# Optimization experiments

Hardware: AMD Instinct MI355X
Metric: run time of the kernel (lower is better)

The kernel has to match this reference:

```python
import jax, jax.numpy as jnp
import numpy as np

NUM_CLASSES = 10

def setup_inputs() -> dict:
    key = jax.random.key(0)
    k1, k2, k3 = jax.random.split(key, 3)
    X = jax.random.normal(k1, (1024, 128), dtype=jnp.float32)
    X_train = jax.random.normal(k2, (100000, 128), dtype=jnp.float32)
    y_train = jax.random.randint(k3, (100000,), 0, NUM_CLASSES, dtype=jnp.int64)
    return {"X": X, "X_train": X_train, "y_train": y_train, "k": 5}


def reference(X, X_train, y_train, k):
    test_sq = jnp.sum(X * X, axis=1, keepdims=True)            # [T, 1]
    train_sq = jnp.sum(X_train * X_train, axis=1)[None, :]     # [1, N]
    cross = X @ X_train.T                                      # [T, N]
    dists = jnp.sqrt(jnp.maximum(test_sq + train_sq - 2.0 * cross, 0.0))
    # top-k nearest: smallest distances == largest negated distances
    _, idx = jax.lax.top_k(-dists, k)                          # [T, k]
    labels = y_train[idx]                                      # [T, k]
    # majority vote; argmax returns the smallest label on ties,
    # matching most_frq_smaller semantics
    counts = jnp.sum(jax.nn.one_hot(labels, NUM_CLASSES, dtype=jnp.int32), axis=1)  # [T, C]
    y_pred = jnp.argmax(counts, axis=1).astype(jnp.float32)    # torch.zeros default float
    return y_pred
```

## Files before the change

kernel.cpp:

```cpp
#include <hip/hip_runtime.h>
#include <cfloat>
#include <cstdint>


#define NTRAIN 100000
#define D 128
#define T 1024
#define TB 128
#define NT 32
#define KNN 5
#define NUM_CLASSES 10
#define NCH 125
#define CHUNK 800
#define NSUB 32
#define SCHUNK 224
#define NTILE_TOT 3125
#define TILE_HALVES 8192

typedef _Float16 half8 __attribute__((ext_vector_type(8)));
typedef float f32x16 __attribute__((ext_vector_type(16)));

#define MFMA(a, b, c) __builtin_amdgcn_mfma_f32_32x32x16_f16((a), (b), (c), 0, 0, 0)

struct Cand { float s; int j; };

__device__ __forceinline__ bool better(float s, int j, const Cand& c) {
    return (s > c.s) || (s == c.s && j < c.j);
}

__device__ __forceinline__ void ins5(Cand t5[KNN], float s, int j) {
    if (!better(s, j, t5[4])) return;
    if (better(s, j, t5[0]))      { t5[4]=t5[3]; t5[3]=t5[2]; t5[2]=t5[1]; t5[1]=t5[0]; t5[0]={s,j}; }
    else if (better(s, j, t5[1])) { t5[4]=t5[3]; t5[3]=t5[2]; t5[2]=t5[1]; t5[1]={s,j}; }
    else if (better(s, j, t5[2])) { t5[4]=t5[3]; t5[3]=t5[2]; t5[2]={s,j}; }
    else if (better(s, j, t5[3])) { t5[4]=t5[3]; t5[3]={s,j}; }
    else                          { t5[4]={s,j}; }
}

__device__ __forceinline__ void gload_lds16(const void* g, void* l) {
    __builtin_amdgcn_global_load_lds(
        (const __attribute__((address_space(1))) uint32_t*)g,
        (__attribute__((address_space(3))) uint32_t*)l, 16, 0, 0);
}

__global__ __launch_bounds__(256)
void knn_norms(const float* __restrict__ XT, uint32_t* __restrict__ nrmp) {
    const int j = blockIdx.x * 256 + threadIdx.x;
    if (j >= NTRAIN) return;
    const float4* row = (const float4*)&XT[(size_t)j * D];
    float p[32];
#pragma unroll
    for (int c = 0; c < 32; ++c) {
        float4 v = row[c];
        p[c] = v.x * v.x + v.y * v.y + v.z * v.z + v.w * v.w;
    }
#pragma unroll
    for (int s = 1; s < 32; s <<= 1)
#pragma unroll
        for (int i = 0; i < 32; i += 2 * s) p[i] += p[i + s];
    const float m = -0.5f * p[0];
    const _Float16 mh = (_Float16)m;
    const _Float16 ml = (_Float16)(m - (float)mh);
    union { _Float16 h[2]; uint32_t u; } cv;
    cv.h[0] = mh; cv.h[1] = ml;
    nrmp[j] = cv.u;
}

__global__ __launch_bounds__(256)
void knn_pack(const float* __restrict__ XT, _Float16* __restrict__ XTs,
              uint32_t* __restrict__ nrmp) {
    __shared__ __align__(16) float sb[32 * D];
    const int tid  = threadIdx.x;
    const int tile = blockIdx.x;
    const float4* src = (const float4*)&XT[(size_t)tile * 32 * D];
#pragma unroll
    for (int p = 0; p < 4; ++p)
        *(float4*)&sb[(p * 256 + tid) * 4] = src[p * 256 + tid];
    __syncthreads();

    {
        const int ks = tid >> 5, kh = (tid >> 4) & 1, rp = (tid & 15) * 2;
        const int c0 = ks * 16 + kh * 8;
        _Float16* outp = &XTs[(size_t)tile * TILE_HALVES + tid * 16];
#pragma unroll
        for (int rr = 0; rr < 2; ++rr) {
            const float* s = &sb[(rp + rr) * D + c0];
            half8 hv, lv;
#pragma unroll
            for (int e = 0; e < 8; ++e) {
                float v = s[e];
                _Float16 hh = (_Float16)v;
                hv[e] = hh; lv[e] = (_Float16)(v - (float)hh);
            }
            *(half8*)&outp[rr * 8]        = hv;
            *(half8*)&outp[4096 + rr * 8] = lv;
        }
    }
    {
        const int row = tid >> 3, seg = tid & 7;
        const float4* rp4 = (const float4*)&sb[row * D];
        float q[4];
#pragma unroll
        for (int c = 0; c < 4; ++c) {
            float4 v = rp4[seg * 4 + c];
            q[c] = v.x * v.x + v.y * v.y + v.z * v.z + v.w * v.w;
        }
        float part = (q[0] + q[1]) + (q[2] + q[3]);
        part += __shfl_xor(part, 1);
        part += __shfl_xor(part, 2);
        part += __shfl_xor(part, 4);
        if (seg == 0) {
            const float m = -0.5f * part;
            const _Float16 mh = (_Float16)m;
            const _Float16 ml = (_Float16)(m - (float)mh);
            union { _Float16 h[2]; uint32_t u; } cv;
            cv.h[0] = mh; cv.h[1] = ml;
            nrmp[tile * 32 + row] = cv.u;
        }
    }
}

template <bool SPLIT, bool THRESH>
__global__ __launch_bounds__(256, 4)
void knn_mfma(const float* __restrict__ X, const float* __restrict__ XT,
              const _Float16* __restrict__ XTs, const uint32_t* __restrict__ nrmp,
              Cand* __restrict__ part, int nch, int chunk,
              const float* __restrict__ thrb, Cand* __restrict__ thrc) {
    __shared__ __align__(16) _Float16 lds[2][TILE_HALVES];

    const int tid  = threadIdx.x;
    const int lane = tid & 63;
    const int wv   = tid >> 6;
    const int bx   = blockIdx.x;
    const int bc   = blockIdx.y;

    half8 Bh[8], Bl[8];
    {
        const int trow = bx * TB + wv * 32 + (lane & 31);
        const float* xp = &X[(size_t)trow * D + (lane >> 5) * 8];
#pragma unroll
        for (int ks = 0; ks < 8; ++ks) {
            float4 v0 = *(const float4*)&xp[ks * 16];
            float4 v1 = *(const float4*)&xp[ks * 16 + 4];
            float a[8] = {v0.x, v0.y, v0.z, v0.w, v1.x, v1.y, v1.z, v1.w};
#pragma unroll
            for (int e = 0; e < 8; ++e) {
                _Float16 hh = (_Float16)a[e];
                Bh[ks][e] = hh;
                Bl[ks][e] = (_Float16)(a[e] - (float)hh);
            }
        }
    }
    half8 B8;
#pragma unroll
    for (int e = 0; e < 8; ++e) B8[e] = (_Float16)0.0f;
    if (lane < 32) B8[0] = (_Float16)1.0f;

    f32x16 kZero;
#pragma unroll
    for (int e = 0; e < 16; ++e) kZero[e] = 0.f;

    const int srow = tid & 31;
    const int ksp  = tid >> 5;
    float a16[16];

    _Float16* const l0 = &lds[0][wv * 512];
    _Float16* const l1 = &lds[1][wv * 512];

    auto issue_stage_split = [&](int buf, const _Float16* g) {
        _Float16* l = buf ? l1 : l0;
#pragma unroll
        for (int p = 0; p < 4; ++p)
            gload_lds16(g + p * 2048, l + p * 2048);
    };
    auto issue_loads = [&](int jb) {
        int j = jb + srow;
        if (j > NTRAIN - 1) j = NTRAIN - 1;
        const float4* p = (const float4*)&XT[(size_t)j * D + ksp * 16];
        float4 v0 = p[0], v1 = p[1], v2 = p[2], v3 = p[3];
        a16[0]=v0.x; a16[1]=v0.y; a16[2]=v0.z; a16[3]=v0.w;
        a16[4]=v1.x; a16[5]=v1.y; a16[6]=v1.z; a16[7]=v1.w;
        a16[8]=v2.x; a16[9]=v2.y; a16[10]=v2.z; a16[11]=v2.w;
        a16[12]=v3.x; a16[13]=v3.y; a16[14]=v3.z; a16[15]=v3.w;
    };
    auto write_stage = [&](int buf) {
        half8 hv0, lv0, hv1, lv1;
#pragma unroll
        for (int e = 0; e < 8; ++e) {
            _Float16 hh = (_Float16)a16[e];
            hv0[e] = hh; lv0[e] = (_Float16)(a16[e] - (float)hh);
        }
#pragma unroll
        for (int e = 0; e < 8; ++e) {
            _Float16 hh = (_Float16)a16[8 + e];
            hv1[e] = hh; lv1[e] = (_Float16)(a16[8 + e] - (float)hh);
        }
        _Float16* base = &lds[buf][ksp * 512 + srow * 8];
        *(half8*)(base)              = hv0;
        *(half8*)(base + 256)        = hv1;
        *(half8*)(base + 4096)       = lv0;
        *(half8*)(base + 4096 + 256) = lv1;
    };

    float s0 = -FLT_MAX;
    if (!THRESH && thrb != nullptr) {
        const int col = bx * TB + wv * 32 + (lane & 31);
        s0 = thrb[col];
    }
    Cand top5[KNN];
#pragma unroll
    for (int e = 0; e < KNN; ++e) top5[e] = {s0, 0x7fffffff};

    const int jc0 = bc * chunk;
    const int ntiles = chunk >> 5;
    const int tile0 = jc0 >> 5;

    const _Float16* gcur = &XTs[(size_t)tile0 * TILE_HALVES + wv * 512 + lane * 8];

    if (SPLIT) {
        issue_stage_split(0, gcur);
    } else {
        issue_loads(jc0);
        write_stage(0);
    }
    __syncthreads();

    for (int t = 0; t < ntiles; ++t) {
        const int jb = jc0 + t * NT;
        if (!SPLIT && jb >= NTRAIN) break;
        const int buf = t & 1;
        const bool more = (t + 1 < ntiles);

        if (SPLIT) {
            gcur += TILE_HALVES;
            if (more) issue_stage_split(buf ^ 1, gcur);
        } else {
            if (more) issue_loads(jb + NT);
        }

        int nj = jb + (lane & 31);
        if (!SPLIT && nj > NTRAIN - 1) nj = NTRAIN - 1;
        uint32_t nv = nrmp[nj];
        if (lane >= 32) nv = 0;

        const _Float16* rbase = &lds[buf][lane * 8];
        __builtin_amdgcn_s_setprio(1);
        f32x16 acc;
        {
            half8 ah = *(const half8*)(rbase);
            half8 al = *(const half8*)(rbase + 4096);
            acc = MFMA(ah, Bh[0], kZero);
            acc = MFMA(ah, Bl[0], acc);
            acc = MFMA(al, Bh[0], acc);
        }
#pragma unroll
        for (int ks = 1; ks < 8; ++ks) {
            half8 ah = *(const half8*)(rbase + ks * 512);
            half8 al = *(const half8*)(rbase + 4096 + ks * 512);
            acc = MFMA(ah, Bh[ks], acc);
            acc = MFMA(ah, Bl[ks], acc);
            acc = MFMA(al, Bh[ks], acc);
        }
        {
            union { uint32_t u; _Float16 h[2]; } cv; cv.u = nv;
            half8 augh, augl;
#pragma unroll
            for (int e = 0; e < 8; ++e) { augh[e] = (_Float16)0.0f; augl[e] = (_Float16)0.0f; }
            augh[0] = cv.h[0];
            augl[0] = cv.h[1];
            acc = MFMA(augh, B8, acc);
            acc = MFMA(augl, B8, acc);
        }
        __builtin_amdgcn_s_setprio(0);

        if (!SPLIT && more) write_stage(buf ^ 1);

        __syncthreads();

        const int rb = 4 * (lane >> 5);
#pragma unroll
        for (int reg = 0; reg < 16; ++reg) {
            const float s = acc[reg];
            if (s >= top5[4].s) {
                const int j = jb + (reg & 3) + 8 * (reg >> 2) + rb;
                if (SPLIT || j < NTRAIN) ins5(top5, s, j);
            }
        }
    }

    {
        float os[KNN]; int oj[KNN];
#pragma unroll
        for (int e = 0; e < KNN; ++e) {
            os[e] = __shfl_xor(top5[e].s, 32);
            oj[e] = __shfl_xor(top5[e].j, 32);
        }
#pragma unroll
        for (int e = 0; e < KNN; ++e) ins5(top5, os[e], oj[e]);
        if (lane < 32) {
            const int test = bx * TB + wv * 32 + lane;
            if (THRESH) {
                Cand* pp = &thrc[((size_t)test * NSUB + bc) * KNN];
#pragma unroll
                for (int e = 0; e < KNN; ++e) pp[e] = top5[e];
            } else {
                Cand* pp = &part[((size_t)test * nch + bc) * KNN];
#pragma unroll
                for (int e = 0; e < KNN; ++e) pp[e] = top5[e];
            }
        }
    }
}

__global__ __launch_bounds__(256)
void knn_thrmerge(const Cand* __restrict__ thrc, float* __restrict__ thr) {
    const int tid  = threadIdx.x;
    const int lane = tid & 63;
    const int test = blockIdx.x * 4 + (tid >> 6);
    if (test >= T) return;

    Cand best[KNN];
#pragma unroll
    for (int e = 0; e < KNN; ++e) best[e] = {-FLT_MAX, 0x7fffffff};

    if (lane < NSUB) {
        const Cand* pp = &thrc[((size_t)test * NSUB + lane) * KNN];
#pragma unroll
        for (int e = 0; e < KNN; ++e) {
            const Cand cc = pp[e];
            if ((unsigned)cc.j < (unsigned)NTRAIN) ins5(best, cc.s, cc.j);
        }
    }
#pragma unroll
    for (int off = 32; off >= 1; off >>= 1) {
        float os[KNN]; int oj[KNN];
#pragma unroll
        for (int e = 0; e < KNN; ++e) {
            os[e] = __shfl_xor(best[e].s, off);
            oj[e] = __shfl_xor(best[e].j, off);
        }
#pragma unroll
        for (int e = 0; e < KNN; ++e)
            if ((unsigned)oj[e] < (unsigned)NTRAIN) ins5(best, os[e], oj[e]);
    }
    if (lane == 0) thr[test] = best[4].s;
}

__global__ __launch_bounds__(256)
void knn_vote2(const Cand* __restrict__ part, const int* __restrict__ y,
               float* __restrict__ out, int nch) {
    const int tid  = threadIdx.x;
    const int lane = tid & 63;
    const int test = blockIdx.x * 4 + (tid >> 6);
    if (test >= T) return;

    Cand best[KNN];
#pragma unroll
    for (int e = 0; e < KNN; ++e) best[e] = {-FLT_MAX, 0x7fffffff};

    for (int c = lane; c < nch; c += 64) {
        const Cand* pp = &part[((size_t)test * nch + c) * KNN];
#pragma unroll
        for (int e = 0; e < KNN; ++e) {
            const Cand cc = pp[e];
            if ((unsigned)cc.j < (unsigned)NTRAIN) ins5(best, cc.s, cc.j);
        }
    }
#pragma unroll
    for (int off = 32; off >= 1; off >>= 1) {
        float os[KNN]; int oj[KNN];
#pragma unroll
        for (int e = 0; e < KNN; ++e) {
            os[e] = __shfl_xor(best[e].s, off);
            oj[e] = __shfl_xor(best[e].j, off);
        }
#pragma unroll
        for (int e = 0; e < KNN; ++e)
            if ((unsigned)oj[e] < (unsigned)NTRAIN) ins5(best, os[e], oj[e]);
    }
    if (lane == 0) {
        int lbl[KNN];
#pragma unroll
        for (int e = 0; e < KNN; ++e) lbl[e] = y[best[e].j];
        int bestc = 0, bestcnt = -1;
#pragma unroll
        for (int c = 0; c < NUM_CLASSES; ++c) {
            int cnt = 0;
#pragma unroll
            for (int e = 0; e < KNN; ++e) cnt += (lbl[e] == c) ? 1 : 0;
            if (cnt > bestcnt) { bestcnt = cnt; bestc = c; }
        }
        out[test] = (float)bestc;
    }
}

extern "C" void kernel_launch(void* const* d_in, const int* in_sizes, int n_in,
                              void* d_out, int out_size, void* d_ws, size_t ws_size,
                              hipStream_t stream) {
    const float* X  = (const float*)d_in[0];
    const float* XT = (const float*)d_in[1];
    const int*   y  = (const int*)d_in[2];

    const size_t xts_bytes  = (size_t)NTILE_TOT * TILE_HALVES * 2;
    const size_t nrm_bytes  = ((size_t)NTRAIN * 4 + 255) & ~(size_t)255;
    const size_t thrc_bytes = ((size_t)T * NSUB * KNN * sizeof(Cand) + 255) & ~(size_t)255;
    const size_t thr_bytes  = ((size_t)T * 4 + 255) & ~(size_t)255;
    const size_t per_chunk  = (size_t)T * KNN * sizeof(Cand);
    const size_t part_bytes = (size_t)NCH * per_chunk;

    const size_t need_full = xts_bytes + nrm_bytes + thrc_bytes + thr_bytes + part_bytes;
    const size_t need_noth = xts_bytes + nrm_bytes + part_bytes;

    if (ws_size >= need_full) {
        _Float16* XTs  = (_Float16*)d_ws;
        uint32_t* nrmp = (uint32_t*)((char*)d_ws + xts_bytes);
        Cand*     thrc = (Cand*)((char*)d_ws + xts_bytes + nrm_bytes);
        float*    thr  = (float*)((char*)d_ws + xts_bytes + nrm_bytes + thrc_bytes);
        Cand*     part = (Cand*)((char*)d_ws + xts_bytes + nrm_bytes + thrc_bytes + thr_bytes);
        knn_pack<<<NTILE_TOT, 256, 0, stream>>>(XT, XTs, nrmp);
        knn_mfma<true, true><<<dim3(T / TB, NSUB), 256, 0, stream>>>(
            X, XT, XTs, nrmp, nullptr, NSUB, SCHUNK, nullptr, thrc);
        knn_thrmerge<<<T / 4, 256, 0, stream>>>(thrc, thr);
        knn_mfma<true, false><<<dim3(T / TB, NCH), 256, 0, stream>>>(
            X, XT, XTs, nrmp, part, NCH, CHUNK, thr, nullptr);
        knn_vote2<<<T / 4, 256, 0, stream>>>(part, y, (float*)d_out, NCH);
    } else if (ws_size >= need_noth) {
        _Float16* XTs  = (_Float16*)d_ws;
        uint32_t* nrmp = (uint32_t*)((char*)d_ws + xts_bytes);
        Cand*     part = (Cand*)((char*)d_ws + xts_bytes + nrm_bytes);
        knn_pack<<<NTILE_TOT, 256, 0, stream>>>(XT, XTs, nrmp);
        knn_mfma<true, false><<<dim3(T / TB, NCH), 256, 0, stream>>>(
            X, XT, XTs, nrmp, part, NCH, CHUNK, nullptr, nullptr);
        knn_vote2<<<T / 4, 256, 0, stream>>>(part, y, (float*)d_out, NCH);
    } else {
        uint32_t* nrmp = (uint32_t*)d_ws;
        Cand*     part = (Cand*)((char*)d_ws + nrm_bytes);
        int fch = NCH;
        if (nrm_bytes + (size_t)fch * per_chunk > ws_size) {
            size_t avail = (ws_size > nrm_bytes) ? (ws_size - nrm_bytes) : 0;
            fch = (int)(avail / per_chunk);
            if (fch < 1) fch = 1;
        }
        const int chunk = (((NTRAIN + fch - 1) / fch) + (NT - 1)) & ~(NT - 1);
        knn_norms<<<(NTRAIN + 255) / 256, 256, 0, stream>>>(XT, nrmp);
        knn_mfma<false, false><<<dim3(T / TB, fch), 256, 0, stream>>>(
            X, XT, nullptr, nrmp, part, fch, chunk, nullptr, nullptr);
        knn_vote2<<<T / 4, 256, 0, stream>>>(part, y, (float*)d_out, fch);
    }
}
```

Before: 169.4 us.

## Remap mfma grid so each XCD owns whole train chunks; pad pack LDS rows

The 2D grid becomes a 1D grid where the low three block-index bits select the XCD. Each XCD then processes all 8 test-row blocks of the same training chunks, so the chunk's packed tiles stay in that XCD's L2 instead of being fetched separately by several dies. Extra blocks from rounding up to a multiple of 64 exit early. Separately, the pack kernel's shared-memory rows are padded from 128 to 132 floats to reduce LDS bank conflicts on the strided reads.

```diff
diff --git a/kernel.cpp b/kernel.cpp
--- a/kernel.cpp
+++ b/kernel.cpp
@@ -16,6 +16,7 @@
 #define SCHUNK 224
 #define NTILE_TOT 3125
 #define TILE_HALVES 8192
+#define SBS 132
 
 typedef _Float16 half8 __attribute__((ext_vector_type(8)));
 typedef float f32x16 __attribute__((ext_vector_type(16)));
@@ -69,13 +70,17 @@
 __global__ __launch_bounds__(256)
 void knn_pack(const float* __restrict__ XT, _Float16* __restrict__ XTs,
               uint32_t* __restrict__ nrmp) {
-    __shared__ __align__(16) float sb[32 * D];
+    __shared__ __align__(16) float sb[32 * SBS];
     const int tid  = threadIdx.x;
     const int tile = blockIdx.x;
     const float4* src = (const float4*)&XT[(size_t)tile * 32 * D];
 #pragma unroll
-    for (int p = 0; p < 4; ++p)
-        *(float4*)&sb[(p * 256 + tid) * 4] = src[p * 256 + tid];
+    for (int p = 0; p < 4; ++p) {
+        const int i4  = p * 256 + tid;
+        const int row = i4 >> 5;
+        const int c4  = i4 & 31;
+        *(float4*)&sb[row * SBS + c4 * 4] = src[i4];
+    }
     __syncthreads();
 
     {
@@ -84,7 +89,7 @@
         _Float16* outp = &XTs[(size_t)tile * TILE_HALVES + tid * 16];
 #pragma unroll
         for (int rr = 0; rr < 2; ++rr) {
-            const float* s = &sb[(rp + rr) * D + c0];
+            const float* s = &sb[(rp + rr) * SBS + c0];
             half8 hv, lv;
 #pragma unroll
             for (int e = 0; e < 8; ++e) {
@@ -98,7 +103,7 @@
     }
     {
         const int row = tid >> 3, seg = tid & 7;
-        const float4* rp4 = (const float4*)&sb[row * D];
+        const float4* rp4 = (const float4*)&sb[row * SBS];
         float q[4];
 #pragma unroll
         for (int c = 0; c < 4; ++c) {
@@ -131,8 +136,13 @@
     const int tid  = threadIdx.x;
     const int lane = tid & 63;
     const int wv   = tid >> 6;
-    const int bx   = blockIdx.x;
-    const int bc   = blockIdx.y;
+
+    const int L   = blockIdx.x;
+    const int xcd = L & 7;
+    const int s_  = L >> 3;
+    const int bx  = s_ & 7;
+    const int bc  = (s_ & ~7) | xcd;
+    if (bc >= nch) return;
 
     half8 Bh[8], Bl[8];
     {
@@ -394,6 +404,10 @@
     }
 }
 
+static inline int grid_for(int nch) {
+    return 8 * (((nch + 7) / 8) * 8);
+}
+
 extern "C" void kernel_launch(void* const* d_in, const int* in_sizes, int n_in,
                               void* d_out, int out_size, void* d_ws, size_t ws_size,
                               hipStream_t stream) {
@@ -418,10 +432,10 @@
         float*    thr  = (float*)((char*)d_ws + xts_bytes + nrm_bytes + thrc_bytes);
         Cand*     part = (Cand*)((char*)d_ws + xts_bytes + nrm_bytes + thrc_bytes + thr_bytes);
         knn_pack<<<NTILE_TOT, 256, 0, stream>>>(XT, XTs, nrmp);
-        knn_mfma<true, true><<<dim3(T / TB, NSUB), 256, 0, stream>>>(
+        knn_mfma<true, true><<<grid_for(NSUB), 256, 0, stream>>>(
             X, XT, XTs, nrmp, nullptr, NSUB, SCHUNK, nullptr, thrc);
         knn_thrmerge<<<T / 4, 256, 0, stream>>>(thrc, thr);
-        knn_mfma<true, false><<<dim3(T / TB, NCH), 256, 0, stream>>>(
+        knn_mfma<true, false><<<grid_for(NCH), 256, 0, stream>>>(
             X, XT, XTs, nrmp, part, NCH, CHUNK, thr, nullptr);
         knn_vote2<<<T / 4, 256, 0, stream>>>(part, y, (float*)d_out, NCH);
     } else if (ws_size >= need_noth) {
@@ -429,7 +443,7 @@
         uint32_t* nrmp = (uint32_t*)((char*)d_ws + xts_bytes);
         Cand*     part = (Cand*)((char*)d_ws + xts_bytes + nrm_bytes);
         knn_pack<<<NTILE_TOT, 256, 0, stream>>>(XT, XTs, nrmp);
-        knn_mfma<true, false><<<dim3(T / TB, NCH), 256, 0, stream>>>(
+        knn_mfma<true, false><<<grid_for(NCH), 256, 0, stream>>>(
             X, XT, XTs, nrmp, part, NCH, CHUNK, nullptr, nullptr);
         knn_vote2<<<T / 4, 256, 0, stream>>>(part, y, (float*)d_out, NCH);
     } else {
@@ -443,7 +457,7 @@
         }
         const int chunk = (((NTRAIN + fch - 1) / fch) + (NT - 1)) & ~(NT - 1);
         knn_norms<<<(NTRAIN + 255) / 256, 256, 0, stream>>>(XT, nrmp);
-        knn_mfma<false, false><<<dim3(T / TB, fch), 256, 0, stream>>>(
+        knn_mfma<false, false><<<grid_for(fch), 256, 0, stream>>>(
             X, XT, nullptr, nrmp, part, fch, chunk, nullptr, nullptr);
         knn_vote2<<<T / 4, 256, 0, stream>>>(part, y, (float*)d_out, fch);
     }
```

Result: faster. 165.6 us (-2.2%).
